# Kernel tuning notes

Hardware: AMD Instinct MI355X
Metric: run time of the kernel (lower is better)

## Reference

```python
import jax, jax.numpy as jnp
import numpy as np

BS, SL, FD = 8192, 49, 11
D_MODEL, DM2, HEAD = 128, 64, 8
NH, NHID, NLAYER = DM2 // HEAD, 4, 2
ABF = 1.0
XY_IDX = np.array([0, 1, 2, 3, 4, 5, 6, 7, 10])  # x feats + y feat (batch-normed cols)
DEC_IN = D_MODEL + 10  # d_model + len(x_dims + spa_dims)


def tanhshrink(x):
    return x - jnp.tanh(x)


def rope_angles(spa):
    # spa: [bs, sl, 2] -> per-token block angles [bs, sl, 4]
    # block order matches torch.block_diag(Rx(t0), Ry(t0), Rx(t1), Ry(t1))
    thetas = 10000.0 ** ((2.0 - 2.0 * jnp.arange(2, dtype=spa.dtype)) / 8.0)  # d=8, n_thetas=2
    ax = spa[..., 0:1] * thetas  # [bs, sl, 2]
    ay = spa[..., 1:2] * thetas
    return jnp.stack([ax[..., 0], ay[..., 0], ax[..., 1], ay[..., 1]], axis=-1)


def apply_rope(v, ang):
    # v: [bs, nh, s, 8]; ang: [bs, s, 4]. Applies the 8x8 block-diagonal
    # rotation directly on 2-d sub-pairs (same math as R @ v, no 8x8 matmats).
    c = jnp.cos(ang)[:, None]  # [bs, 1, s, 4]
    s = jnp.sin(ang)[:, None]
    v2 = v.reshape(*v.shape[:-1], 4, 2)
    r = jnp.stack([c * v2[..., 0] - s * v2[..., 1],
                   s * v2[..., 0] + c * v2[..., 1]], axis=-1)
    return r.reshape(v.shape)


def heads(x):  # [bs, s, dm2] -> [bs, nh, s, hd]
    b, s, _ = x.shape
    return x.reshape(b, s, NH, HEAD).transpose(0, 2, 1, 3)


def merge(x):  # [bs, nh, s, hd] -> [bs, s, dm2]
    b, h, s, d = x.shape
    return x.transpose(0, 2, 1, 3).reshape(b, s, h * d)


def mlp2(x, w1, b1, w2, b2):
    return tanhshrink(x @ w1 + b1) @ w2 + b2


def forward_impl(input_tensor, dists, bn_gamma, bn_beta,
                 xe_w1, xe_b1, xe_w2, xe_b2, ye_w1, ye_b1, ye_w2, ye_b2,
                 learnable_y, hidden_tokens, Wq, Wk, Wv, Wo, Wq2, Wk2, Wv2, Wo2,
                 dec_w0, dec_b0, dec_w1, dec_b1, dec_w2, dec_b2):
    bs = input_tensor.shape[0]
    # --- NanBatchNorm over x+y feature columns (no NaNs in clean inputs) ---
    xy = input_tensor[:, :, XY_IDX]
    mu = jnp.mean(xy, axis=(0, 1), keepdims=True)
    var = jnp.var(xy, axis=(0, 1), keepdims=True)
    xy = (xy - mu) / jnp.sqrt(var + 1e-5) * bn_gamma + bn_beta
    input_tensor = input_tensor.at[:, :, XY_IDX].set(xy)

    # --- target at last seq position: drop its dist, keep context dists ---
    dists_ctx = dists[:, :-1]                       # [bs, sl-1]
    central_x = input_tensor[:, -1:, :-1]           # [bs, 1, 10] (x + spa feats)

    # --- 2D RoPE angles from spatial coords ---
    ang = rope_angles(input_tensor[:, :, 8:10])     # [bs, sl, 4]

    # --- FCN encoders (two streams a=x, b=y) ---
    x_embed = mlp2(input_tensor[:, :, :8], xe_w1, xe_b1, xe_w2, xe_b2)      # [bs, sl, 64]
    y_embed = mlp2(input_tensor[:, :-1, 10:11], ye_w1, ye_b1, ye_w2, ye_b2)  # [bs, sl-1, 64]
    y_embed = jnp.concatenate([y_embed, jnp.broadcast_to(learnable_y, (bs, 1, DM2))], axis=1)

    ctx = (x_embed[:, :-1], y_embed[:, :-1])
    qry = (x_embed[:, -1:], y_embed[:, -1:])
    ang_ctx, ang_q = ang[:, :-1], ang[:, -1:]
    bias = (-ABF * dists_ctx)[:, None, None, :]     # [bs, 1, 1, sl-1]
    scale = 1.0 / jnp.sqrt(jnp.asarray(HEAD, input_tensor.dtype))

    outs, attn_ws = [], []
    for s in range(2):
        H = jnp.broadcast_to(hidden_tokens, (bs, NHID, DM2))
        for l in range(NLAYER):
            q = heads(H @ Wq[l, s])
            k = apply_rope(heads(ctx[s] @ Wk[l, s]), ang_ctx)
            v = heads(ctx[s] @ Wv[l, s])
            sc = jnp.einsum('bhqd,bhkd->bhqk', q, k) * scale + bias
            a = jax.nn.softmax(sc, axis=-1)
            H = H + merge(jnp.einsum('bhqk,bhkd->bhqd', a, v)) @ Wo[l, s]
        # query cross-attends the inducing tokens
        q = apply_rope(heads(qry[s] @ Wq2[s]), ang_q)
        k = heads(H @ Wk2[s])
        v = heads(H @ Wv2[s])
        sc = jnp.einsum('bhqd,bhkd->bhqk', q, k) * scale
        a = jax.nn.softmax(sc, axis=-1)
        outs.append(merge(jnp.einsum('bhqk,bhkd->bhqd', a, v)) @ Wo2[s])  # [bs, 1, 64]
        attn_ws.append(a)

    encoding = jnp.concatenate(outs, axis=-1)               # [bs, 1, 128]
    encoding = jnp.concatenate([encoding, central_x], axis=-1)  # [bs, 1, 138]
    h = tanhshrink(encoding @ dec_w0 + dec_b0)
    h = tanhshrink(h @ dec_w1 + dec_b1)
    pred = h @ dec_w2 + dec_b2                              # [bs, 1, 1]
    return pred


def setup_inputs() -> dict:
    key = jax.random.key(0)
    ks = jax.random.split(key, 32)
    g = lambda i, shape: 0.05 * jax.random.normal(ks[i], shape, dtype=jnp.float32)
    inp = {
        'input_tensor': jax.random.normal(ks[0], (BS, SL, FD), dtype=jnp.float32),
        'dists': jax.random.uniform(ks[1], (BS, SL), dtype=jnp.float32),
        'target_position': jnp.zeros((3, BS), dtype=jnp.int32),
        'bn_gamma': jnp.ones((9,), jnp.float32),
        'bn_beta': jnp.zeros((9,), jnp.float32),
        'xe_w1': g(2, (8, DM2)), 'xe_b1': jnp.zeros((DM2,), jnp.float32),
        'xe_w2': g(3, (DM2, DM2)), 'xe_b2': jnp.zeros((DM2,), jnp.float32),
        'ye_w1': g(4, (1, DM2)), 'ye_b1': jnp.zeros((DM2,), jnp.float32),
        'ye_w2': g(5, (DM2, DM2)), 'ye_b2': jnp.zeros((DM2,), jnp.float32),
        'learnable_y': g(6, (1, 1, DM2)),
        'hidden_tokens': g(7, (NHID, DM2)),
        'Wq': g(8, (NLAYER, 2, DM2, DM2)), 'Wk': g(9, (NLAYER, 2, DM2, DM2)),
        'Wv': g(10, (NLAYER, 2, DM2, DM2)), 'Wo': g(11, (NLAYER, 2, DM2, DM2)),
        'Wq2': g(12, (2, DM2, DM2)), 'Wk2': g(13, (2, DM2, DM2)),
        'Wv2': g(14, (2, DM2, DM2)), 'Wo2': g(15, (2, DM2, DM2)),
        'dec_w0': g(16, (DEC_IN, 512)), 'dec_b0': jnp.zeros((512,), jnp.float32),
        'dec_w1': g(17, (512, 256)), 'dec_b1': jnp.zeros((256,), jnp.float32),
        'dec_w2': g(18, (256, 1)), 'dec_b2': jnp.zeros((1,), jnp.float32),
    }
    return inp


def reference(input_tensor, dists, target_position, bn_gamma, bn_beta,
              xe_w1, xe_b1, xe_w2, xe_b2, ye_w1, ye_b1, ye_w2, ye_b2,
              learnable_y, hidden_tokens, Wq, Wk, Wv, Wo, Wq2, Wk2, Wv2, Wo2,
              dec_w0, dec_b0, dec_w1, dec_b1, dec_w2, dec_b2):
    # target_position is an index constant (query is the last token by construction)
    return forward_impl(input_tensor, dists, bn_gamma, bn_beta,
                        xe_w1, xe_b1, xe_w2, xe_b2, ye_w1, ye_b1, ye_w2, ye_b2,
                        learnable_y, hidden_tokens, Wq, Wk, Wv, Wo, Wq2, Wk2, Wv2, Wo2,
                        dec_w0, dec_b0, dec_w1, dec_b1, dec_w2, dec_b2)
```

## Files before the change

### kernel.cpp

```cpp
#include <hip/hip_runtime.h>
#include <math.h>

#define BS 8192
#define SL 49
#define FDIM 11
#define ROWS (BS*SL)

__device__ __forceinline__ float tanhshrink_f(float x) {
  float e = __expf(2.f * x);
  return (x - 1.f) + __fdividef(2.f, e + 1.f);
}

__global__ __launch_bounds__(256) void k_stats(const float* __restrict__ inp,
                                               double* __restrict__ gsum) {
  const int nblk = gridDim.x;
  const int per = (ROWS + nblk - 1) / nblk;
  const int r0 = blockIdx.x * per;
  int r1 = r0 + per; if (r1 > ROWS) r1 = ROWS;
  float s[9], q[9];
#pragma unroll
  for (int j = 0; j < 9; ++j) { s[j] = 0.f; q[j] = 0.f; }
  for (int r = r0 + threadIdx.x; r < r1; r += 256) {
    const float* row = inp + r * FDIM;
#pragma unroll
    for (int j = 0; j < 9; ++j) {
      float v = row[j < 8 ? j : 10];
      s[j] += v; q[j] += v * v;
    }
  }
#pragma unroll
  for (int j = 0; j < 9; ++j) {
    for (int off = 32; off; off >>= 1) {
      s[j] += __shfl_down(s[j], off);
      q[j] += __shfl_down(q[j], off);
    }
  }
  __shared__ float red[4][18];
  const int wid = threadIdx.x >> 6;
  const int lane = threadIdx.x & 63;
  if (lane == 0) {
#pragma unroll
    for (int j = 0; j < 9; ++j) { red[wid][j] = s[j]; red[wid][9 + j] = q[j]; }
  }
  __syncthreads();
  if (threadIdx.x < 18) {
    float t = red[0][threadIdx.x] + red[1][threadIdx.x] +
              red[2][threadIdx.x] + red[3][threadIdx.x];
    atomicAdd(&gsum[threadIdx.x], (double)t);
  }
}

__global__ __launch_bounds__(256) void k_finalize(const double* __restrict__ gsum,
                           const float* __restrict__ gamma,
                           const float* __restrict__ beta,
                           const float* __restrict__ hidden,
                           const float* __restrict__ Wq,
                           const float* __restrict__ xe_w1,
                           const float* __restrict__ xe_w2,
                           const float* __restrict__ ye_w2,
                           const float* __restrict__ Wk,
                           float* __restrict__ bnp,
                           float* __restrict__ q0g,
                           float* __restrict__ xw1T,
                           float* __restrict__ we2,
                           float* __restrict__ wk4) {
  int tid = threadIdx.x;
  if (tid < 9) {
    const double N = (double)ROWS;
    double mean = gsum[tid] / N;
    double msq  = gsum[9 + tid] / N;
    float var = (float)(msq - mean * mean);
    float sc = gamma[tid] / sqrtf(var + 1e-5f);
    bnp[tid] = sc;
    bnp[9 + tid] = beta[tid] - (float)mean * sc;
  }
  int s = tid >> 7, i2 = (tid >> 6) & 1, c = tid & 63;
  const float* W = Wq + (s << 12);
#pragma unroll
  for (int ii = 0; ii < 2; ++ii) {
    int i = i2 + 2 * ii;
    float a = 0.f;
    for (int k = 0; k < 64; ++k) a += hidden[i * 64 + k] * W[k * 64 + c];
    q0g[s * 256 + i * 64 + c] = a;
  }
  for (int i = tid; i < 512; i += 256)  { int cc = i >> 3, k = i & 7; xw1T[i] = xe_w1[k * 64 + cc]; }
  for (int i = tid; i < 8192; i += 256) {
    int ss = i >> 12, r = i & 4095, kc = r >> 8, cc = (r >> 2) & 63, kk = r & 3;
    const float* W2 = ss ? ye_w2 : xe_w2;
    we2[i] = W2[(4 * kc + kk) * 64 + cc];
  }
  for (int i = tid; i < 16384; i += 256) {
    int ls = i >> 12, r = i & 4095, kc = r >> 8, cc = (r >> 2) & 63, kk = r & 3;
    wk4[i] = Wk[ls * 4096 + (4 * kc + kk) * 64 + cc];
  }
}

__global__ __launch_bounds__(256, 4) void k_mega(
    const float* __restrict__ inp, const float* __restrict__ dists,
    const float* __restrict__ bnp, const float* __restrict__ q0g,
    const float* __restrict__ xw1T, const float* __restrict__ xe_b1,
    const float* __restrict__ we2, const float* __restrict__ xe_b2,
    const float* __restrict__ ye_w1, const float* __restrict__ ye_b1,
    const float* __restrict__ ye_b2,
    const float* __restrict__ learnable_y, const float* __restrict__ hidden_tokens,
    const float* __restrict__ Wq, const float* __restrict__ wk4,
    const float* __restrict__ Wv, const float* __restrict__ Wo,
    const float* __restrict__ Wq2, const float* __restrict__ Wk2,
    const float* __restrict__ Wv2, const float* __restrict__ Wo2,
    float* __restrict__ enc)
{
  __shared__ float raw[49][12];
  __shared__ float cs8T[8][52];
  __shared__ float embs[49 * 68];
  __shared__ float KB[49][68];
  __shared__ float scb[32][52];
  __shared__ float Hs[4][64];
  __shared__ float qb[4][64];
  __shared__ float db[48];
  __shared__ float bnl[18];
  __shared__ float q2[64];
  __shared__ float o1[64];
  __shared__ float a2[32];

  const int tid  = threadIdx.x;
  const int lane = tid & 63;
  const int grp  = tid >> 6;
  const int wg   = __builtin_amdgcn_readfirstlane(grp);
  const int b    = blockIdx.x >> 1;
  const int s    = blockIdx.x & 1;
  const float scale = 0.35355339059327373f;

  for (int i = tid; i < 49 * FDIM; i += 256) raw[i / FDIM][i % FDIM] = inp[b * (49*FDIM) + i];
  if (tid < 18) bnl[tid] = bnp[tid];
  if (tid >= 64 && tid < 112) db[tid - 64] = dists[b * 49 + (tid - 64)];
  __syncthreads();

  if (tid < 49) {
    float x = raw[tid][8], y = raw[tid][9];
    cs8T[0][tid] = cosf(10.f * x); cs8T[1][tid] = cosf(10.f * y);
    cs8T[2][tid] = cosf(x);        cs8T[3][tid] = cosf(y);
    cs8T[4][tid] = sinf(10.f * x); cs8T[5][tid] = sinf(10.f * y);
    cs8T[6][tid] = sinf(x);        cs8T[7][tid] = sinf(y);
  }
  for (int i = tid; i < 441; i += 256) {
    int t = i / 9, j = i - t * 9;
    int f = (j < 8) ? j : 10;
    raw[t][f] = raw[t][f] * bnl[j] + bnl[9 + j];
  }
  __syncthreads();

  if (s == 0 && tid < 10) enc[b * 138 + 128 + tid] = raw[48][tid];

  if (s == 0) {
    if (lane < 49) {
      float4 r0 = *(const float4*)&raw[lane][0];
      float4 r1 = *(const float4*)&raw[lane][4];
      const float* w = xw1T + wg * 128;
      float h[16];
#pragma unroll
      for (int ci = 0; ci < 16; ++ci) {
        float a = xe_b1[wg * 16 + ci]
                + r0.x * w[ci*8+0] + r0.y * w[ci*8+1] + r0.z * w[ci*8+2] + r0.w * w[ci*8+3]
                + r1.x * w[ci*8+4] + r1.y * w[ci*8+5] + r1.z * w[ci*8+6] + r1.w * w[ci*8+7];
        h[ci] = tanhshrink_f(a);
      }
#pragma unroll
      for (int i = 0; i < 4; ++i)
        *(float4*)&KB[lane][wg * 16 + 4 * i] = make_float4(h[4*i], h[4*i+1], h[4*i+2], h[4*i+3]);
    }
  } else {
    if (lane < 48) {
      float ry = raw[lane][10];
      float h[16];
#pragma unroll
      for (int ci = 0; ci < 16; ++ci)
        h[ci] = tanhshrink_f(ry * ye_w1[wg * 16 + ci] + ye_b1[wg * 16 + ci]);
#pragma unroll
      for (int i = 0; i < 4; ++i)
        *(float4*)&KB[lane][wg * 16 + 4 * i] = make_float4(h[4*i], h[4*i+1], h[4*i+2], h[4*i+3]);
    }
  }
  __syncthreads();

  {
    const int nrow = (s == 0) ? 49 : 48;
    const float* WE = we2 + (s << 12);
    const float* bb = (s == 0) ? xe_b2 : ye_b2;
    if (lane < nrow) {
      float o[16];
#pragma unroll
      for (int ci = 0; ci < 16; ++ci) o[ci] = bb[wg * 16 + ci];
      for (int kc = 0; kc < 16; ++kc) {
        float4 e = *(const float4*)&KB[lane][kc * 4];
        const float* w = WE + (kc << 8) + (wg << 6);
#pragma unroll
        for (int ci = 0; ci < 16; ++ci)
          o[ci] += e.x * w[ci*4+0] + e.y * w[ci*4+1] + e.z * w[ci*4+2] + e.w * w[ci*4+3];
      }
#pragma unroll
      for (int i = 0; i < 4; ++i)
        *(float4*)&embs[lane * 68 + wg * 16 + 4 * i] = make_float4(o[4*i], o[4*i+1], o[4*i+2], o[4*i+3]);
    }
    if (s == 1 && tid < 64) embs[48 * 68 + lane] = learnable_y[lane];
  }
  Hs[grp][lane] = hidden_tokens[grp * 64 + lane];
  __syncthreads();

#pragma unroll 1
  for (int l = 0; l < 2; ++l) {
    const float* Wv_p = Wv + ((l * 2 + s) << 12);
    const float* Wo_p = Wo + ((l * 2 + s) << 12);
    if (l == 0) {
      qb[grp][lane] = q0g[s * 256 + tid];
    } else {
      const float* Wq_p = Wq + ((l * 2 + s) << 12);
      float a = 0.f;
      for (int k = 0; k < 64; k += 4) {
        float4 hv = *(const float4*)&Hs[grp][k];
        a += hv.x * Wq_p[(k + 0) * 64 + lane] + hv.y * Wq_p[(k + 1) * 64 + lane]
           + hv.z * Wq_p[(k + 2) * 64 + lane] + hv.w * Wq_p[(k + 3) * 64 + lane];
      }
      qb[grp][lane] = a;
    }
    if (lane < 48) {
      float o[16];
#pragma unroll
      for (int ci = 0; ci < 16; ++ci) o[ci] = 0.f;
      const float* WK = wk4 + ((l * 2 + s) << 12);
      for (int kc = 0; kc < 16; ++kc) {
        float4 e = *(const float4*)&embs[lane * 68 + kc * 4];
        const float* w = WK + (kc << 8) + (wg << 6);
#pragma unroll
        for (int ci = 0; ci < 16; ++ci)
          o[ci] += e.x * w[ci*4+0] + e.y * w[ci*4+1] + e.z * w[ci*4+2] + e.w * w[ci*4+3];
      }
      float ko[16];
#pragma unroll
      for (int i = 0; i < 8; ++i) {
        int p = i & 3;
        float co = cs8T[p][lane], si = cs8T[4 + p][lane];
        ko[2*i]   = co * o[2*i] - si * o[2*i+1];
        ko[2*i+1] = si * o[2*i] + co * o[2*i+1];
      }
#pragma unroll
      for (int i = 0; i < 4; ++i)
        *(float4*)&KB[lane][wg * 16 + 4 * i] = make_float4(ko[4*i], ko[4*i+1], ko[4*i+2], ko[4*i+3]);
    }
    __syncthreads();
    {
      const int t0 = tid & 7;
      const int i  = (tid >> 3) & 3;
      const int h  = tid >> 5;
      const int r  = tid >> 3;
      float4 qa = *(const float4*)&qb[i][h * 8];
      float4 qc = *(const float4*)&qb[i][h * 8 + 4];
      float v[6];
#pragma unroll
      for (int j = 0; j < 6; ++j) {
        int t = t0 + 8 * j;
        float4 ka = *(const float4*)&KB[t][h * 8];
        float4 kc = *(const float4*)&KB[t][h * 8 + 4];
        float a = qa.x * ka.x + qa.y * ka.y + qa.z * ka.z + qa.w * ka.w
                + qc.x * kc.x + qc.y * kc.y + qc.z * kc.z + qc.w * kc.w;
        v[j] = a * scale - db[t];
      }
      float m = fmaxf(fmaxf(fmaxf(v[0], v[1]), fmaxf(v[2], v[3])), fmaxf(v[4], v[5]));
      m = fmaxf(m, __shfl_xor(m, 1));
      m = fmaxf(m, __shfl_xor(m, 2));
      m = fmaxf(m, __shfl_xor(m, 4));
      float sum = 0.f;
#pragma unroll
      for (int j = 0; j < 6; ++j) { v[j] = __expf(v[j] - m); sum += v[j]; }
      sum += __shfl_xor(sum, 1);
      sum += __shfl_xor(sum, 2);
      sum += __shfl_xor(sum, 4);
      float inv = 1.f / sum;
#pragma unroll
      for (int j = 0; j < 6; ++j) scb[r][t0 + 8 * j] = v[j] * inv;
    }
    __syncthreads();
    {
      float acc[8];
#pragma unroll
      for (int m = 0; m < 8; ++m) acc[m] = 0.f;
      for (int tt = 0; tt < 48; tt += 4) {
        float e0 = embs[(tt + 0) * 68 + lane], e1 = embs[(tt + 1) * 68 + lane];
        float e2 = embs[(tt + 2) * 68 + lane], e3 = embs[(tt + 3) * 68 + lane];
#pragma unroll
        for (int m = 0; m < 8; ++m) {
          float4 sc4 = *(const float4*)&scb[grp + 4 * m][tt];
          acc[m] += sc4.x * e0 + sc4.y * e1 + sc4.z * e2 + sc4.w * e3;
        }
      }
#pragma unroll
      for (int m = 0; m < 8; ++m) KB[grp + 4 * m][lane] = acc[m];
    }
    {
      const int r = ((lane >> 3) << 2) + grp;
      float a = 0.f;
      for (int c = 0; c < 64; c += 4) {
        float4 tv = *(const float4*)&KB[r][c];
        a += tv.x * Wv_p[(c + 0) * 64 + lane] + tv.y * Wv_p[(c + 1) * 64 + lane]
           + tv.z * Wv_p[(c + 2) * 64 + lane] + tv.w * Wv_p[(c + 3) * 64 + lane];
      }
      qb[grp][lane] = a;
    }
    {
      float a = Hs[grp][lane];
      for (int k = 0; k < 64; k += 4) {
        float4 av = *(const float4*)&qb[grp][k];
        a += av.x * Wo_p[(k + 0) * 64 + lane] + av.y * Wo_p[(k + 1) * 64 + lane]
           + av.z * Wo_p[(k + 2) * 64 + lane] + av.w * Wo_p[(k + 3) * 64 + lane];
      }
      Hs[grp][lane] = a;
    }
    if (l == 0) __syncthreads();
  }

  const float* Wq2_p = Wq2 + (s << 12);
  const float* Wk2_p = Wk2 + (s << 12);
  const float* Wv2_p = Wv2 + (s << 12);
  const float* Wo2_p = Wo2 + (s << 12);
  if (tid < 64) {
    float a = 0.f;
    for (int k = 0; k < 64; k += 4) {
      float4 cv = *(const float4*)&embs[48 * 68 + k];
      a += cv.x * Wq2_p[(k + 0) * 64 + lane] + cv.y * Wq2_p[(k + 1) * 64 + lane]
         + cv.z * Wq2_p[(k + 2) * 64 + lane] + cv.w * Wq2_p[(k + 3) * 64 + lane];
    }
    float other = __shfl_xor(a, 1);
    int p = (lane >> 1) & 3;
    float co = cs8T[p][48], si = cs8T[4 + p][48];
    q2[lane] = (lane & 1) ? (si * other + co * a) : (co * a - si * other);
  }
  {
    float aK = 0.f, aV = 0.f;
    for (int k = 0; k < 64; k += 4) {
      float4 hv = *(const float4*)&Hs[grp][k];
      aK += hv.x * Wk2_p[(k + 0) * 64 + lane] + hv.y * Wk2_p[(k + 1) * 64 + lane]
          + hv.z * Wk2_p[(k + 2) * 64 + lane] + hv.w * Wk2_p[(k + 3) * 64 + lane];
      aV += hv.x * Wv2_p[(k + 0) * 64 + lane] + hv.y * Wv2_p[(k + 1) * 64 + lane]
          + hv.z * Wv2_p[(k + 2) * 64 + lane] + hv.w * Wv2_p[(k + 3) * 64 + lane];
    }
    KB[grp][lane] = aK;
    KB[8 + grp][lane] = aV;
  }
  __syncthreads();
  if (tid < 32) {
    int h = tid >> 2, i = tid & 3;
    float a = 0.f;
#pragma unroll
    for (int d = 0; d < 8; ++d) a += q2[h * 8 + d] * KB[i][h * 8 + d];
    a *= scale;
    float m = fmaxf(a, __shfl_xor(a, 1));
    m = fmaxf(m, __shfl_xor(m, 2));
    float e = __expf(a - m);
    float sum = e + __shfl_xor(e, 1);
    sum += __shfl_xor(sum, 2);
    a2[tid] = e / sum;
  }
  if (tid < 64) {
    int h = lane >> 3;
    float a = 0.f;
#pragma unroll
    for (int i = 0; i < 4; ++i) a += a2[h * 4 + i] * KB[8 + i][lane];
    o1[lane] = a;
  }
  if (tid < 64) {
    float a = 0.f;
    for (int k = 0; k < 64; k += 4) {
      float4 ov = *(const float4*)&o1[k];
      a += ov.x * Wo2_p[(k + 0) * 64 + lane] + ov.y * Wo2_p[(k + 1) * 64 + lane]
         + ov.z * Wo2_p[(k + 2) * 64 + lane] + ov.w * Wo2_p[(k + 3) * 64 + lane];
    }
    enc[b * 138 + s * 64 + lane] = a;
  }
}

__global__ __launch_bounds__(256, 5) void k_dec(
    const float* __restrict__ enc,
    const float* __restrict__ w0, const float* __restrict__ b0,
    const float* __restrict__ w1, const float* __restrict__ b1,
    const float* __restrict__ w2, const float* __restrict__ b2,
    float* __restrict__ out)
{
  __shared__ float encs[8][140];
  __shared__ float h0s[8][512];
  __shared__ float h1s[8][256];
  const int tid = threadIdx.x;
  const int rb = blockIdx.x * 8;

  for (int i = tid; i < 8 * 138; i += 256) {
    int r = i / 138, k = i - r * 138;
    encs[r][k] = enc[(rb + r) * 138 + k];
  }
  __syncthreads();
  {
    float acc0[8], acc1[8];
    const float bb0 = b0[tid], bb1 = b0[tid + 256];
#pragma unroll
    for (int r = 0; r < 8; ++r) { acc0[r] = bb0; acc1[r] = bb1; }
    for (int k = 0; k < 136; k += 4) {
      float wa0 = w0[(k + 0) * 512 + tid], wa1 = w0[(k + 1) * 512 + tid];
      float wa2 = w0[(k + 2) * 512 + tid], wa3 = w0[(k + 3) * 512 + tid];
      float wb0 = w0[(k + 0) * 512 + tid + 256], wb1 = w0[(k + 1) * 512 + tid + 256];
      float wb2 = w0[(k + 2) * 512 + tid + 256], wb3 = w0[(k + 3) * 512 + tid + 256];
#pragma unroll
      for (int r = 0; r < 8; ++r) {
        float4 ev = *(const float4*)&encs[r][k];
        acc0[r] += ev.x * wa0 + ev.y * wa1 + ev.z * wa2 + ev.w * wa3;
        acc1[r] += ev.x * wb0 + ev.y * wb1 + ev.z * wb2 + ev.w * wb3;
      }
    }
    for (int k = 136; k < 138; ++k) {
      float wa = w0[k * 512 + tid], wb = w0[k * 512 + tid + 256];
#pragma unroll
      for (int r = 0; r < 8; ++r) {
        float e = encs[r][k];
        acc0[r] += e * wa; acc1[r] += e * wb;
      }
    }
#pragma unroll
    for (int r = 0; r < 8; ++r) {
      h0s[r][tid] = tanhshrink_f(acc0[r]);
      h0s[r][tid + 256] = tanhshrink_f(acc1[r]);
    }
  }
  __syncthreads();
  {
    float acc[8];
    const float bb = b1[tid];
#pragma unroll
    for (int r = 0; r < 8; ++r) acc[r] = bb;
    for (int k = 0; k < 512; k += 4) {
      float ww0 = w1[(k + 0) * 256 + tid], ww1 = w1[(k + 1) * 256 + tid];
      float ww2 = w1[(k + 2) * 256 + tid], ww3 = w1[(k + 3) * 256 + tid];
#pragma unroll
      for (int r = 0; r < 8; ++r) {
        float4 hv = *(const float4*)&h0s[r][k];
        acc[r] += hv.x * ww0 + hv.y * ww1 + hv.z * ww2 + hv.w * ww3;
      }
    }
#pragma unroll
    for (int r = 0; r < 8; ++r) h1s[r][tid] = tanhshrink_f(acc[r]);
  }
  __syncthreads();
  {
    int r = tid >> 5, l32 = tid & 31;
    float a = 0.f;
#pragma unroll
    for (int kk = 0; kk < 8; ++kk) {
      int k = l32 + 32 * kk;
      a += h1s[r][k] * w2[k];
    }
    for (int off = 16; off; off >>= 1) a += __shfl_down(a, off, 32);
    if (l32 == 0) out[rb + r] = a + b2[0];
  }
}

extern "C" void kernel_launch(void* const* d_in, const int* in_sizes, int n_in,
                              void* d_out, int out_size, void* d_ws, size_t ws_size,
                              hipStream_t stream) {
  const float* inp        = (const float*)d_in[0];
  const float* dists      = (const float*)d_in[1];
  const float* bn_gamma   = (const float*)d_in[3];
  const float* bn_beta    = (const float*)d_in[4];
  const float* xe_w1      = (const float*)d_in[5];
  const float* xe_b1      = (const float*)d_in[6];
  const float* xe_w2      = (const float*)d_in[7];
  const float* xe_b2      = (const float*)d_in[8];
  const float* ye_w1      = (const float*)d_in[9];
  const float* ye_b1      = (const float*)d_in[10];
  const float* ye_w2      = (const float*)d_in[11];
  const float* ye_b2      = (const float*)d_in[12];
  const float* learnable  = (const float*)d_in[13];
  const float* hidden     = (const float*)d_in[14];
  const float* Wq         = (const float*)d_in[15];
  const float* Wk         = (const float*)d_in[16];
  const float* Wv         = (const float*)d_in[17];
  const float* Wo         = (const float*)d_in[18];
  const float* Wq2        = (const float*)d_in[19];
  const float* Wk2        = (const float*)d_in[20];
  const float* Wv2        = (const float*)d_in[21];
  const float* Wo2        = (const float*)d_in[22];
  const float* dec_w0     = (const float*)d_in[23];
  const float* dec_b0     = (const float*)d_in[24];
  const float* dec_w1     = (const float*)d_in[25];
  const float* dec_b1     = (const float*)d_in[26];
  const float* dec_w2     = (const float*)d_in[27];
  const float* dec_b2     = (const float*)d_in[28];

  double* gsum = (double*)d_ws;
  float*  bnp  = (float*)((char*)d_ws + 256);
  float*  q0g  = (float*)((char*)d_ws + 512);
  float*  enc  = (float*)((char*)d_ws + 2560);
  float*  xw1T = (float*)((char*)d_ws + 4524544);
  float*  we2  = (float*)((char*)d_ws + 4526592);
  float*  wk4  = (float*)((char*)d_ws + 4559360);

  hipMemsetAsync(d_ws, 0, 256, stream);
  k_stats   <<<512, 256, 0, stream>>>(inp, gsum);
  k_finalize<<<1, 256, 0, stream>>>(gsum, bn_gamma, bn_beta, hidden, Wq,
                                    xe_w1, xe_w2, ye_w2, Wk,
                                    bnp, q0g, xw1T, we2, wk4);
  k_mega    <<<BS * 2, 256, 0, stream>>>(inp, dists, bnp, q0g,
                                         xw1T, xe_b1, we2, xe_b2,
                                         ye_w1, ye_b1, ye_b2,
                                         learnable, hidden,
                                         Wq, wk4, Wv, Wo, Wq2, Wk2, Wv2, Wo2, enc);
  k_dec     <<<BS / 8, 256, 0, stream>>>(enc, dec_w0, dec_b0, dec_w1, dec_b1,
                                         dec_w2, dec_b2, (float*)d_out);
}
```

Before: 871.5 us.

## Use packed FP32 FMA across encoder and decoder dot products; split weight packing kernel

Rewrites the many scalar FMA chains in the mega and decoder kernels as two-wide vector FMAs, aiming for packed FP32 instructions that do two multiply-adds per issue, with the two halves summed at the end. Weight repacking moves out of the single-block finalize kernel into a separate 32-block kernel so it runs with more parallelism. Costs are extra operand packing moves, changed summation order, and possibly higher register pressure.

```diff
diff --git a/kernel.cpp b/kernel.cpp
--- a/kernel.cpp
+++ b/kernel.cpp
@@ -5,6 +5,13 @@
 #define SL 49
 #define FDIM 11
 #define ROWS (BS*SL)
+
+typedef float v2f __attribute__((ext_vector_type(2)));
+
+__device__ __forceinline__ v2f mk2(float a, float b) { v2f r; r.x = a; r.y = b; return r; }
+__device__ __forceinline__ v2f pkfma(v2f a, v2f b, v2f c) {
+  return __builtin_elementwise_fma(a, b, c);
+}
 
 __device__ __forceinline__ float tanhshrink_f(float x) {
   float e = __expf(2.f * x);
@@ -50,20 +57,34 @@
   }
 }
 
+__global__ __launch_bounds__(256) void k_pack(const float* __restrict__ xe_w1,
+                          const float* __restrict__ xe_w2,
+                          const float* __restrict__ ye_w2,
+                          const float* __restrict__ Wk,
+                          float* __restrict__ xw1T,
+                          float* __restrict__ we2,
+                          float* __restrict__ wk4) {
+  int gid = blockIdx.x * 256 + threadIdx.x;
+  if (gid < 512) { int cc = gid >> 3, k = gid & 7; xw1T[gid] = xe_w1[k * 64 + cc]; }
+  {
+    int i = gid;
+    int ss = i >> 12, r = i & 4095, kc = r >> 8, cc = (r >> 2) & 63, kk = r & 3;
+    const float* W2 = ss ? ye_w2 : xe_w2;
+    we2[i] = W2[(4 * kc + kk) * 64 + cc];
+  }
+  for (int i = gid; i < 16384; i += 8192) {
+    int ls = i >> 12, r = i & 4095, kc = r >> 8, cc = (r >> 2) & 63, kk = r & 3;
+    wk4[i] = Wk[ls * 4096 + (4 * kc + kk) * 64 + cc];
+  }
+}
+
 __global__ __launch_bounds__(256) void k_finalize(const double* __restrict__ gsum,
                            const float* __restrict__ gamma,
                            const float* __restrict__ beta,
                            const float* __restrict__ hidden,
                            const float* __restrict__ Wq,
-                           const float* __restrict__ xe_w1,
-                           const float* __restrict__ xe_w2,
-                           const float* __restrict__ ye_w2,
-                           const float* __restrict__ Wk,
                            float* __restrict__ bnp,
-                           float* __restrict__ q0g,
-                           float* __restrict__ xw1T,
-                           float* __restrict__ we2,
-                           float* __restrict__ wk4) {
+                           float* __restrict__ q0g) {
   int tid = threadIdx.x;
   if (tid < 9) {
     const double N = (double)ROWS;
@@ -82,16 +103,6 @@
     float a = 0.f;
     for (int k = 0; k < 64; ++k) a += hidden[i * 64 + k] * W[k * 64 + c];
     q0g[s * 256 + i * 64 + c] = a;
-  }
-  for (int i = tid; i < 512; i += 256)  { int cc = i >> 3, k = i & 7; xw1T[i] = xe_w1[k * 64 + cc]; }
-  for (int i = tid; i < 8192; i += 256) {
-    int ss = i >> 12, r = i & 4095, kc = r >> 8, cc = (r >> 2) & 63, kk = r & 3;
-    const float* W2 = ss ? ye_w2 : xe_w2;
-    we2[i] = W2[(4 * kc + kk) * 64 + cc];
-  }
-  for (int i = tid; i < 16384; i += 256) {
-    int ls = i >> 12, r = i & 4095, kc = r >> 8, cc = (r >> 2) & 63, kk = r & 3;
-    wk4[i] = Wk[ls * 4096 + (4 * kc + kk) * 64 + cc];
   }
 }
 
@@ -159,10 +170,12 @@
       float h[16];
 #pragma unroll
       for (int ci = 0; ci < 16; ++ci) {
-        float a = xe_b1[wg * 16 + ci]
-                + r0.x * w[ci*8+0] + r0.y * w[ci*8+1] + r0.z * w[ci*8+2] + r0.w * w[ci*8+3]
-                + r1.x * w[ci*8+4] + r1.y * w[ci*8+5] + r1.z * w[ci*8+6] + r1.w * w[ci*8+7];
-        h[ci] = tanhshrink_f(a);
+        v2f h2 = mk2(0.f, 0.f);
+        h2 = pkfma(mk2(r0.x, r0.y), *(const v2f*)&w[ci*8+0], h2);
+        h2 = pkfma(mk2(r0.z, r0.w), *(const v2f*)&w[ci*8+2], h2);
+        h2 = pkfma(mk2(r1.x, r1.y), *(const v2f*)&w[ci*8+4], h2);
+        h2 = pkfma(mk2(r1.z, r1.w), *(const v2f*)&w[ci*8+6], h2);
+        h[ci] = tanhshrink_f(xe_b1[wg * 16 + ci] + h2.x + h2.y);
       }
 #pragma unroll
       for (int i = 0; i < 4; ++i)
@@ -187,16 +200,22 @@
     const float* WE = we2 + (s << 12);
     const float* bb = (s == 0) ? xe_b2 : ye_b2;
     if (lane < nrow) {
-      float o[16];
-#pragma unroll
-      for (int ci = 0; ci < 16; ++ci) o[ci] = bb[wg * 16 + ci];
+      v2f o2[16];
+#pragma unroll
+      for (int ci = 0; ci < 16; ++ci) o2[ci] = mk2(0.f, 0.f);
       for (int kc = 0; kc < 16; ++kc) {
         float4 e = *(const float4*)&KB[lane][kc * 4];
         const float* w = WE + (kc << 8) + (wg << 6);
-#pragma unroll
-        for (int ci = 0; ci < 16; ++ci)
-          o[ci] += e.x * w[ci*4+0] + e.y * w[ci*4+1] + e.z * w[ci*4+2] + e.w * w[ci*4+3];
-      }
+        v2f exy = mk2(e.x, e.y), ezw = mk2(e.z, e.w);
+#pragma unroll
+        for (int ci = 0; ci < 16; ++ci) {
+          o2[ci] = pkfma(exy, *(const v2f*)&w[ci*4+0], o2[ci]);
+          o2[ci] = pkfma(ezw, *(const v2f*)&w[ci*4+2], o2[ci]);
+        }
+      }
+      float o[16];
+#pragma unroll
+      for (int ci = 0; ci < 16; ++ci) o[ci] = bb[wg * 16 + ci] + o2[ci].x + o2[ci].y;
 #pragma unroll
       for (int i = 0; i < 4; ++i)
         *(float4*)&embs[lane * 68 + wg * 16 + 4 * i] = make_float4(o[4*i], o[4*i+1], o[4*i+2], o[4*i+3]);
@@ -214,26 +233,34 @@
       qb[grp][lane] = q0g[s * 256 + tid];
     } else {
       const float* Wq_p = Wq + ((l * 2 + s) << 12);
-      float a = 0.f;
+      v2f a2v = mk2(0.f, 0.f);
       for (int k = 0; k < 64; k += 4) {
         float4 hv = *(const float4*)&Hs[grp][k];
-        a += hv.x * Wq_p[(k + 0) * 64 + lane] + hv.y * Wq_p[(k + 1) * 64 + lane]
-           + hv.z * Wq_p[(k + 2) * 64 + lane] + hv.w * Wq_p[(k + 3) * 64 + lane];
-      }
-      qb[grp][lane] = a;
+        float w0 = Wq_p[(k + 0) * 64 + lane], w1 = Wq_p[(k + 1) * 64 + lane];
+        float w2 = Wq_p[(k + 2) * 64 + lane], w3 = Wq_p[(k + 3) * 64 + lane];
+        a2v = pkfma(mk2(hv.x, hv.y), mk2(w0, w1), a2v);
+        a2v = pkfma(mk2(hv.z, hv.w), mk2(w2, w3), a2v);
+      }
+      qb[grp][lane] = a2v.x + a2v.y;
     }
     if (lane < 48) {
-      float o[16];
-#pragma unroll
-      for (int ci = 0; ci < 16; ++ci) o[ci] = 0.f;
+      v2f o2[16];
+#pragma unroll
+      for (int ci = 0; ci < 16; ++ci) o2[ci] = mk2(0.f, 0.f);
       const float* WK = wk4 + ((l * 2 + s) << 12);
       for (int kc = 0; kc < 16; ++kc) {
         float4 e = *(const float4*)&embs[lane * 68 + kc * 4];
         const float* w = WK + (kc << 8) + (wg << 6);
-#pragma unroll
-        for (int ci = 0; ci < 16; ++ci)
-          o[ci] += e.x * w[ci*4+0] + e.y * w[ci*4+1] + e.z * w[ci*4+2] + e.w * w[ci*4+3];
-      }
+        v2f exy = mk2(e.x, e.y), ezw = mk2(e.z, e.w);
+#pragma unroll
+        for (int ci = 0; ci < 16; ++ci) {
+          o2[ci] = pkfma(exy, *(const v2f*)&w[ci*4+0], o2[ci]);
+          o2[ci] = pkfma(ezw, *(const v2f*)&w[ci*4+2], o2[ci]);
+        }
+      }
+      float o[16];
+#pragma unroll
+      for (int ci = 0; ci < 16; ++ci) o[ci] = o2[ci].x + o2[ci].y;
       float ko[16];
 #pragma unroll
       for (int i = 0; i < 8; ++i) {
@@ -260,9 +287,12 @@
         int t = t0 + 8 * j;
         float4 ka = *(const float4*)&KB[t][h * 8];
         float4 kc = *(const float4*)&KB[t][h * 8 + 4];
-        float a = qa.x * ka.x + qa.y * ka.y + qa.z * ka.z + qa.w * ka.w
-                + qc.x * kc.x + qc.y * kc.y + qc.z * kc.z + qc.w * kc.w;
-        v[j] = a * scale - db[t];
+        v2f d2 = mk2(0.f, 0.f);
+        d2 = pkfma(mk2(qa.x, qa.y), mk2(ka.x, ka.y), d2);
+        d2 = pkfma(mk2(qa.z, qa.w), mk2(ka.z, ka.w), d2);
+        d2 = pkfma(mk2(qc.x, qc.y), mk2(kc.x, kc.y), d2);
+        d2 = pkfma(mk2(qc.z, qc.w), mk2(kc.z, kc.w), d2);
+        v[j] = (d2.x + d2.y) * scale - db[t];
       }
       float m = fmaxf(fmaxf(fmaxf(v[0], v[1]), fmaxf(v[2], v[3])), fmaxf(v[4], v[5]));
       m = fmaxf(m, __shfl_xor(m, 1));
@@ -280,39 +310,45 @@
     }
     __syncthreads();
     {
-      float acc[8];
-#pragma unroll
-      for (int m = 0; m < 8; ++m) acc[m] = 0.f;
+      v2f acc2[8];
+#pragma unroll
+      for (int m = 0; m < 8; ++m) acc2[m] = mk2(0.f, 0.f);
       for (int tt = 0; tt < 48; tt += 4) {
         float e0 = embs[(tt + 0) * 68 + lane], e1 = embs[(tt + 1) * 68 + lane];
         float e2 = embs[(tt + 2) * 68 + lane], e3 = embs[(tt + 3) * 68 + lane];
+        v2f e01 = mk2(e0, e1), e23 = mk2(e2, e3);
 #pragma unroll
         for (int m = 0; m < 8; ++m) {
           float4 sc4 = *(const float4*)&scb[grp + 4 * m][tt];
-          acc[m] += sc4.x * e0 + sc4.y * e1 + sc4.z * e2 + sc4.w * e3;
+          acc2[m] = pkfma(mk2(sc4.x, sc4.y), e01, acc2[m]);
+          acc2[m] = pkfma(mk2(sc4.z, sc4.w), e23, acc2[m]);
         }
       }
 #pragma unroll
-      for (int m = 0; m < 8; ++m) KB[grp + 4 * m][lane] = acc[m];
+      for (int m = 0; m < 8; ++m) KB[grp + 4 * m][lane] = acc2[m].x + acc2[m].y;
     }
     {
       const int r = ((lane >> 3) << 2) + grp;
-      float a = 0.f;
+      v2f a2v = mk2(0.f, 0.f);
       for (int c = 0; c < 64; c += 4) {
         float4 tv = *(const float4*)&KB[r][c];
-        a += tv.x * Wv_p[(c + 0) * 64 + lane] + tv.y * Wv_p[(c + 1) * 64 + lane]
-           + tv.z * Wv_p[(c + 2) * 64 + lane] + tv.w * Wv_p[(c + 3) * 64 + lane];
-      }
-      qb[grp][lane] = a;
+        float w0 = Wv_p[(c + 0) * 64 + lane], w1 = Wv_p[(c + 1) * 64 + lane];
+        float w2 = Wv_p[(c + 2) * 64 + lane], w3 = Wv_p[(c + 3) * 64 + lane];
+        a2v = pkfma(mk2(tv.x, tv.y), mk2(w0, w1), a2v);
+        a2v = pkfma(mk2(tv.z, tv.w), mk2(w2, w3), a2v);
+      }
+      qb[grp][lane] = a2v.x + a2v.y;
     }
     {
-      float a = Hs[grp][lane];
+      v2f a2v = mk2(Hs[grp][lane], 0.f);
       for (int k = 0; k < 64; k += 4) {
         float4 av = *(const float4*)&qb[grp][k];
-        a += av.x * Wo_p[(k + 0) * 64 + lane] + av.y * Wo_p[(k + 1) * 64 + lane]
-           + av.z * Wo_p[(k + 2) * 64 + lane] + av.w * Wo_p[(k + 3) * 64 + lane];
-      }
-      Hs[grp][lane] = a;
+        float w0 = Wo_p[(k + 0) * 64 + lane], w1 = Wo_p[(k + 1) * 64 + lane];
+        float w2 = Wo_p[(k + 2) * 64 + lane], w3 = Wo_p[(k + 3) * 64 + lane];
+        a2v = pkfma(mk2(av.x, av.y), mk2(w0, w1), a2v);
+        a2v = pkfma(mk2(av.z, av.w), mk2(w2, w3), a2v);
+      }
+      Hs[grp][lane] = a2v.x + a2v.y;
     }
     if (l == 0) __syncthreads();
   }
@@ -322,28 +358,36 @@
   const float* Wv2_p = Wv2 + (s << 12);
   const float* Wo2_p = Wo2 + (s << 12);
   if (tid < 64) {
-    float a = 0.f;
+    v2f a2v = mk2(0.f, 0.f);
     for (int k = 0; k < 64; k += 4) {
       float4 cv = *(const float4*)&embs[48 * 68 + k];
-      a += cv.x * Wq2_p[(k + 0) * 64 + lane] + cv.y * Wq2_p[(k + 1) * 64 + lane]
-         + cv.z * Wq2_p[(k + 2) * 64 + lane] + cv.w * Wq2_p[(k + 3) * 64 + lane];
-    }
+      float w0 = Wq2_p[(k + 0) * 64 + lane], w1 = Wq2_p[(k + 1) * 64 + lane];
+      float w2 = Wq2_p[(k + 2) * 64 + lane], w3 = Wq2_p[(k + 3) * 64 + lane];
+      a2v = pkfma(mk2(cv.x, cv.y), mk2(w0, w1), a2v);
+      a2v = pkfma(mk2(cv.z, cv.w), mk2(w2, w3), a2v);
+    }
+    float a = a2v.x + a2v.y;
     float other = __shfl_xor(a, 1);
     int p = (lane >> 1) & 3;
     float co = cs8T[p][48], si = cs8T[4 + p][48];
     q2[lane] = (lane & 1) ? (si * other + co * a) : (co * a - si * other);
   }
   {
-    float aK = 0.f, aV = 0.f;
+    v2f aK2 = mk2(0.f, 0.f), aV2 = mk2(0.f, 0.f);
     for (int k = 0; k < 64; k += 4) {
       float4 hv = *(const float4*)&Hs[grp][k];
-      aK += hv.x * Wk2_p[(k + 0) * 64 + lane] + hv.y * Wk2_p[(k + 1) * 64 + lane]
-          + hv.z * Wk2_p[(k + 2) * 64 + lane] + hv.w * Wk2_p[(k + 3) * 64 + lane];
-      aV += hv.x * Wv2_p[(k + 0) * 64 + lane] + hv.y * Wv2_p[(k + 1) * 64 + lane]
-          + hv.z * Wv2_p[(k + 2) * 64 + lane] + hv.w * Wv2_p[(k + 3) * 64 + lane];
-    }
-    KB[grp][lane] = aK;
-    KB[8 + grp][lane] = aV;
+      v2f hxy = mk2(hv.x, hv.y), hzw = mk2(hv.z, hv.w);
+      float k0 = Wk2_p[(k + 0) * 64 + lane], k1 = Wk2_p[(k + 1) * 64 + lane];
+      float k2 = Wk2_p[(k + 2) * 64 + lane], k3 = Wk2_p[(k + 3) * 64 + lane];
+      float v0 = Wv2_p[(k + 0) * 64 + lane], v1 = Wv2_p[(k + 1) * 64 + lane];
+      float v2 = Wv2_p[(k + 2) * 64 + lane], v3 = Wv2_p[(k + 3) * 64 + lane];
+      aK2 = pkfma(hxy, mk2(k0, k1), aK2);
+      aK2 = pkfma(hzw, mk2(k2, k3), aK2);
+      aV2 = pkfma(hxy, mk2(v0, v1), aV2);
+      aV2 = pkfma(hzw, mk2(v2, v3), aV2);
+    }
+    KB[grp][lane] = aK2.x + aK2.y;
+    KB[8 + grp][lane] = aV2.x + aV2.y;
   }
   __syncthreads();
   if (tid < 32) {
@@ -367,13 +411,15 @@
     o1[lane] = a;
   }
   if (tid < 64) {
-    float a = 0.f;
+    v2f a2v = mk2(0.f, 0.f);
     for (int k = 0; k < 64; k += 4) {
       float4 ov = *(const float4*)&o1[k];
-      a += ov.x * Wo2_p[(k + 0) * 64 + lane] + ov.y * Wo2_p[(k + 1) * 64 + lane]
-         + ov.z * Wo2_p[(k + 2) * 64 + lane] + ov.w * Wo2_p[(k + 3) * 64 + lane];
-    }
-    enc[b * 138 + s * 64 + lane] = a;
+      float w0 = Wo2_p[(k + 0) * 64 + lane], w1 = Wo2_p[(k + 1) * 64 + lane];
+      float w2 = Wo2_p[(k + 2) * 64 + lane], w3 = Wo2_p[(k + 3) * 64 + lane];
+      a2v = pkfma(mk2(ov.x, ov.y), mk2(w0, w1), a2v);
+      a2v = pkfma(mk2(ov.z, ov.w), mk2(w2, w3), a2v);
+    }
+    enc[b * 138 + s * 64 + lane] = a2v.x + a2v.y;
   }
 }
 
@@ -396,53 +442,63 @@
   }
   __syncthreads();
   {
-    float acc0[8], acc1[8];
-    const float bb0 = b0[tid], bb1 = b0[tid + 256];
-#pragma unroll
-    for (int r = 0; r < 8; ++r) { acc0[r] = bb0; acc1[r] = bb1; }
+    v2f acc0[8], acc1[8];
+#pragma unroll
+    for (int r = 0; r < 8; ++r) { acc0[r] = mk2(0.f, 0.f); acc1[r] = mk2(0.f, 0.f); }
     for (int k = 0; k < 136; k += 4) {
       float wa0 = w0[(k + 0) * 512 + tid], wa1 = w0[(k + 1) * 512 + tid];
       float wa2 = w0[(k + 2) * 512 + tid], wa3 = w0[(k + 3) * 512 + tid];
       float wb0 = w0[(k + 0) * 512 + tid + 256], wb1 = w0[(k + 1) * 512 + tid + 256];
       float wb2 = w0[(k + 2) * 512 + tid + 256], wb3 = w0[(k + 3) * 512 + tid + 256];
+      v2f wa01 = mk2(wa0, wa1), wa23 = mk2(wa2, wa3);
+      v2f wb01 = mk2(wb0, wb1), wb23 = mk2(wb2, wb3);
 #pragma unroll
       for (int r = 0; r < 8; ++r) {
         float4 ev = *(const float4*)&encs[r][k];
-        acc0[r] += ev.x * wa0 + ev.y * wa1 + ev.z * wa2 + ev.w * wa3;
-        acc1[r] += ev.x * wb0 + ev.y * wb1 + ev.z * wb2 + ev.w * wb3;
-      }
-    }
+        v2f exy = mk2(ev.x, ev.y), ezw = mk2(ev.z, ev.w);
+        acc0[r] = pkfma(exy, wa01, acc0[r]);
+        acc0[r] = pkfma(ezw, wa23, acc0[r]);
+        acc1[r] = pkfma(exy, wb01, acc1[r]);
+        acc1[r] = pkfma(ezw, wb23, acc1[r]);
+      }
+    }
+    const float bb0 = b0[tid], bb1 = b0[tid + 256];
+    float t0[8], t1[8];
+#pragma unroll
+    for (int r = 0; r < 8; ++r) { t0[r] = bb0 + acc0[r].x + acc0[r].y; t1[r] = bb1 + acc1[r].x + acc1[r].y; }
     for (int k = 136; k < 138; ++k) {
       float wa = w0[k * 512 + tid], wb = w0[k * 512 + tid + 256];
 #pragma unroll
       for (int r = 0; r < 8; ++r) {
         float e = encs[r][k];
-        acc0[r] += e * wa; acc1[r] += e * wb;
+        t0[r] += e * wa; t1[r] += e * wb;
       }
     }
 #pragma unroll
     for (int r = 0; r < 8; ++r) {
-      h0s[r][tid] = tanhshrink_f(acc0[r]);
-      h0s[r][tid + 256] = tanhshrink_f(acc1[r]);
+      h0s[r][tid] = tanhshrink_f(t0[r]);
+      h0s[r][tid + 256] = tanhshrink_f(t1[r]);
     }
   }
   __syncthreads();
   {
-    float acc[8];
-    const float bb = b1[tid];
-#pragma unroll
-    for (int r = 0; r < 8; ++r) acc[r] = bb;
+    v2f acc[8];
+#pragma unroll
+    for (int r = 0; r < 8; ++r) acc[r] = mk2(0.f, 0.f);
     for (int k = 0; k < 512; k += 4) {
       float ww0 = w1[(k + 0) * 256 + tid], ww1 = w1[(k + 1) * 256 + tid];
       float ww2 = w1[(k + 2) * 256 + tid], ww3 = w1[(k + 3) * 256 + tid];
+      v2f w01 = mk2(ww0, ww1), w23 = mk2(ww2, ww3);
 #pragma unroll
       for (int r = 0; r < 8; ++r) {
         float4 hv = *(const float4*)&h0s[r][k];
-        acc[r] += hv.x * ww0 + hv.y * ww1 + hv.z * ww2 + hv.w * ww3;
-      }
-    }
-#pragma unroll
-    for (int r = 0; r < 8; ++r) h1s[r][tid] = tanhshrink_f(acc[r]);
+        acc[r] = pkfma(mk2(hv.x, hv.y), w01, acc[r]);
+        acc[r] = pkfma(mk2(hv.z, hv.w), w23, acc[r]);
+      }
+    }
+    const float bb = b1[tid];
+#pragma unroll
+    for (int r = 0; r < 8; ++r) h1s[r][tid] = tanhshrink_f(bb + acc[r].x + acc[r].y);
   }
   __syncthreads();
   {
@@ -499,10 +555,9 @@
   float*  wk4  = (float*)((char*)d_ws + 4559360);
 
   hipMemsetAsync(d_ws, 0, 256, stream);
+  k_pack    <<<32, 256, 0, stream>>>(xe_w1, xe_w2, ye_w2, Wk, xw1T, we2, wk4);
   k_stats   <<<512, 256, 0, stream>>>(inp, gsum);
-  k_finalize<<<1, 256, 0, stream>>>(gsum, bn_gamma, bn_beta, hidden, Wq,
-                                    xe_w1, xe_w2, ye_w2, Wk,
-                                    bnp, q0g, xw1T, we2, wk4);
+  k_finalize<<<1, 256, 0, stream>>>(gsum, bn_gamma, bn_beta, hidden, Wq, bnp, q0g);
   k_mega    <<<BS * 2, 256, 0, stream>>>(inp, dists, bnp, q0g,
                                          xw1T, xe_b1, we2, xe_b2,
                                          ye_w1, ye_b1, ye_b2,
```

Result: slower. 941.0 us (+8.0%).
